# Optimization experiments

Measured on AMD Instinct MI355X. Metric: run time of the kernel, lower is better.

Reference implementation:

```python
import jax, jax.numpy as jnp
import numpy as np

V, D, L, H, T_BLK, DFF = 50257, 768, 12, 12, 1024, 4096
DK = D // H
LN_EPS = 1e-5


def setup_inputs() -> dict:
    key = jax.random.key(0)
    ks = jax.random.split(key, 16)
    s = 0.02
    inp = {
        "idx": jax.random.randint(ks[0], (2, 1024), 0, V),
        "tok_emb": jax.random.normal(ks[1], (V, D), jnp.float32) * s,
        "pos_emb": jax.random.normal(ks[2], (1, T_BLK, D), jnp.float32) * s,
        "ln1_w": jnp.ones((L, D), jnp.float32),
        "ln1_b": jnp.zeros((L, D), jnp.float32),
        "qkv_w": jax.random.normal(ks[3], (L, 3 * D, D), jnp.float32) * s,
        "qkv_b": jnp.zeros((L, 3 * D), jnp.float32),
        "proj_w": jax.random.normal(ks[4], (L, D, D), jnp.float32) * s,
        "proj_b": jnp.zeros((L, D), jnp.float32),
        "ln2_w": jnp.ones((L, D), jnp.float32),
        "ln2_b": jnp.zeros((L, D), jnp.float32),
        "ff1_w": jax.random.normal(ks[5], (L, DFF, D), jnp.float32) * s,
        "ff1_b": jnp.zeros((L, DFF), jnp.float32),
        "ff2_w": jax.random.normal(ks[6], (L, D, DFF), jnp.float32) * s,
        "ff2_b": jnp.zeros((L, D), jnp.float32),
        "lnf_w": jnp.ones((D,), jnp.float32),
        "lnf_b": jnp.zeros((D,), jnp.float32),
        "head_w": jax.random.normal(ks[7], (V, D), jnp.float32) * s,
    }
    return inp


def _layernorm(x, w, b):
    mu = jnp.mean(x, axis=-1, keepdims=True)
    var = jnp.var(x, axis=-1, keepdims=True)
    return (x - mu) * jax.lax.rsqrt(var + LN_EPS) * w + b


def _gpt_forward(idx, tok_emb, pos_emb, ln1_w, ln1_b, qkv_w, qkv_b, proj_w, proj_b,
                 ln2_w, ln2_b, ff1_w, ff1_b, ff2_w, ff2_b, lnf_w, lnf_b, head_w):
    B, T = idx.shape
    x = tok_emb[idx] + pos_emb[:, :T, :]  # [B,T,D]
    mask = jnp.tril(jnp.ones((T, T), bool))  # causal
    scale = 1.0 / np.sqrt(DK)

    def step(x, p):
        l1w, l1b, qw, qb, pw, pb, l2w, l2b, f1w, f1b, f2w, f2b = p
        h = _layernorm(x, l1w, l1b)
        qkv = h @ qw.T + qb  # [B,T,3D]
        q, k, v = jnp.split(qkv, 3, axis=-1)
        q = q.reshape(B, T, H, DK).transpose(0, 2, 1, 3)  # [B,H,T,DK]
        k = k.reshape(B, T, H, DK).transpose(0, 2, 1, 3)
        v = v.reshape(B, T, H, DK).transpose(0, 2, 1, 3)
        att = jnp.einsum('bhtd,bhsd->bhts', q, k) * scale
        att = jnp.where(mask, att, -jnp.inf)
        att = jax.nn.softmax(att, axis=-1)
        y = jnp.einsum('bhts,bhsd->bhtd', att, v)
        y = y.transpose(0, 2, 1, 3).reshape(B, T, D)
        x = x + y @ pw.T + pb
        h2 = _layernorm(x, l2w, l2b)
        ff = jax.nn.gelu(h2 @ f1w.T + f1b, approximate=False) @ f2w.T + f2b
        return x + ff, None

    params = (ln1_w, ln1_b, qkv_w, qkv_b, proj_w, proj_b,
              ln2_w, ln2_b, ff1_w, ff1_b, ff2_w, ff2_b)
    x, _ = jax.lax.scan(step, x, params)
    x = _layernorm(x, lnf_w, lnf_b)
    return x @ head_w.T  # [B,T,V] logits


def reference(idx, tok_emb, pos_emb, ln1_w, ln1_b, qkv_w, qkv_b, proj_w, proj_b,
              ln2_w, ln2_b, ff1_w, ff1_b, ff2_w, ff2_b, lnf_w, lnf_b, head_w):
    return _gpt_forward(idx, tok_emb, pos_emb, ln1_w, ln1_b, qkv_w, qkv_b, proj_w,
                        proj_b, ln2_w, ln2_b, ff1_w, ff1_b, ff2_w, ff2_b,
                        lnf_w, lnf_b, head_w)
```

## Files before the change

### kernel.cpp

```cpp
#include <hip/hip_runtime.h>
#include <hip/hip_bf16.h>
#include <math.h>

#define Dm 768
#define Tt 1024
#define Bb 2
#define Hh 12
#define DFF 4096
#define Ll 12
#define Vv 50257
#define ROWS (Bb*Tt)
#define LN_EPS 1e-5f

typedef unsigned int uint;
typedef unsigned short ushort;
typedef float f32x4 __attribute__((ext_vector_type(4)));
typedef short bf16x8 __attribute__((ext_vector_type(8)));
typedef ushort us8 __attribute__((ext_vector_type(8)));

__device__ __forceinline__ ushort f2bf(float f) {
  uint u = __builtin_bit_cast(uint, f);
  u += 0x7FFFu + ((u >> 16) & 1u);
  return (ushort)(u >> 16);
}

#define GLL(gp, lp)                                                          \
  __builtin_amdgcn_global_load_lds(                                          \
      (const __attribute__((address_space(1))) uint*)(gp),                   \
      (__attribute__((address_space(3))) uint*)(lp), 16, 0, 0)

__global__ __launch_bounds__(256) void embed_ln(
    const int* __restrict__ idx, const float* __restrict__ tok,
    const float* __restrict__ pos, const float* __restrict__ w,
    const float* __restrict__ b, float* __restrict__ x,
    ushort* __restrict__ out) {
  const int row = blockIdx.x;
  const int t = row & (Tt - 1);
  const int tid = threadIdx.x;
  const float* tsrc = tok + (size_t)idx[row] * Dm;
  const float* psrc = pos + (size_t)t * Dm;
  float v[3];
  float sum = 0.f, sq = 0.f;
#pragma unroll
  for (int i = 0; i < 3; i++) {
    const int d = tid + i * 256;
    v[i] = tsrc[d] + psrc[d];
    x[(size_t)row * Dm + d] = v[i];
    sum += v[i]; sq += v[i] * v[i];
  }
#pragma unroll
  for (int off = 32; off > 0; off >>= 1) {
    sum += __shfl_xor(sum, off);
    sq  += __shfl_xor(sq, off);
  }
  __shared__ float red[8];
  const int wid = tid >> 6, lane = tid & 63;
  if (lane == 0) { red[wid] = sum; red[wid + 4] = sq; }
  __syncthreads();
  sum = red[0] + red[1] + red[2] + red[3];
  sq  = red[4] + red[5] + red[6] + red[7];
  const float mu = sum * (1.f / Dm);
  const float var = sq * (1.f / Dm) - mu * mu;
  const float rstd = rsqrtf(var + LN_EPS);
  ushort* dst = out + (size_t)row * Dm;
#pragma unroll
  for (int i = 0; i < 3; i++) {
    const int d = tid + i * 256;
    dst[d] = f2bf((v[i] - mu) * rstd * w[d] + b[d]);
  }
}

__global__ __launch_bounds__(192) void red_ln(
    const float* __restrict__ part, int nsk, const float* __restrict__ bias,
    float* __restrict__ x, const float* __restrict__ w,
    const float* __restrict__ b, ushort* __restrict__ out) {
  const int row = blockIdx.x;
  const int tid = threadIdx.x;
  const size_t o4 = (size_t)row * 192 + tid;
  float4 xv = ((const float4*)x)[o4];
  const float4 b4 = ((const float4*)bias)[tid];
  xv.x += b4.x; xv.y += b4.y; xv.z += b4.z; xv.w += b4.w;
  for (int k = 0; k < nsk; k++) {
    const float4 p = ((const float4*)part)[(size_t)k * ROWS * 192 + o4];
    xv.x += p.x; xv.y += p.y; xv.z += p.z; xv.w += p.w;
  }
  ((float4*)x)[o4] = xv;
  float sum = xv.x + xv.y + xv.z + xv.w;
  float sq = xv.x * xv.x + xv.y * xv.y + xv.z * xv.z + xv.w * xv.w;
#pragma unroll
  for (int off = 32; off > 0; off >>= 1) {
    sum += __shfl_xor(sum, off);
    sq  += __shfl_xor(sq, off);
  }
  __shared__ float red[6];
  const int wid = tid >> 6, lane = tid & 63;
  if (lane == 0) { red[wid] = sum; red[wid + 3] = sq; }
  __syncthreads();
  sum = red[0] + red[1] + red[2];
  sq  = red[3] + red[4] + red[5];
  const float mu = sum * (1.f / Dm);
  const float var = sq * (1.f / Dm) - mu * mu;
  const float rstd = rsqrtf(var + LN_EPS);
  const float4 w4 = ((const float4*)w)[tid];
  const float4 bb4 = ((const float4*)b)[tid];
  ushort4 o;
  o.x = f2bf((xv.x - mu) * rstd * w4.x + bb4.x);
  o.y = f2bf((xv.y - mu) * rstd * w4.y + bb4.y);
  o.z = f2bf((xv.z - mu) * rstd * w4.z + bb4.z);
  o.w = f2bf((xv.w - mu) * rstd * w4.w + bb4.w);
  ((ushort4*)out)[o4] = o;
}

__global__ __launch_bounds__(256) void convert_w(
    const float* __restrict__ s, ushort* __restrict__ d, int n4) {
  const int stride = gridDim.x * 256;
  for (int i = blockIdx.x * 256 + threadIdx.x; i < n4; i += stride) {
    const float4 v = ((const float4*)s)[i];
    ushort4 o;
    o.x = f2bf(v.x); o.y = f2bf(v.y); o.z = f2bf(v.z); o.w = f2bf(v.w);
    ((ushort4*)d)[i] = o;
  }
}

#define EPI_QKV 0
#define EPI_PART 1
#define EPI_BIAS_GELU 2
#define EPI_NONE 3

template <int EPI>
__global__ __launch_bounds__(256) void gemm_mfma(
    const ushort* __restrict__ A, const ushort* __restrict__ B,
    const float* __restrict__ bias, void* __restrict__ Cv,
    void* __restrict__ Cv2, int Kloop, int Kstr, int Nloc, int ldC) {
  __shared__ char lds[32768];
  const int tid = threadIdx.x;
  const int l = tid & 63;
  const int wid = __builtin_amdgcn_readfirstlane(tid >> 6);
  const int wr = wid >> 1, wc = wid & 1;
  const int m0 = blockIdx.y * 128;
  const int n0 = blockIdx.x * 128;
  const int z = (EPI == EPI_PART) ? blockIdx.z : 0;
  if (EPI == EPI_PART) { A += (size_t)z * Kloop; B += (size_t)z * Kloop; }

  const int cperm = (((l & 3) ^ ((l >> 3) & 3)) * 8);
  const ushort* gA = A + (size_t)(m0 + wid * 32 + (l >> 2)) * Kstr + cperm;
  int rB = n0 + wid * 32 + (l >> 2);
  rB = min(rB, Nloc - 1);
  const ushort* gB = B + (size_t)rB * Kstr + cperm;

  const int rdSw = (l & 15) * 64 + (((l >> 4) ^ ((l >> 1) & 3)) * 16);
  const int aRd = wr * 4096 + rdSw;
  const int bRd = 8192 + wc * 4096 + rdSw;

  f32x4 acc[4][4] = {};
  const int nt = Kloop / 32;

  {
    const int lb = wid * 2048;
    GLL(gA, lds + lb);          GLL(gA + 16 * Kstr, lds + lb + 1024);
    GLL(gB, lds + 8192 + lb);   GLL(gB + 16 * Kstr, lds + 8192 + lb + 1024);
  }

  for (int t = 0; t < nt; ++t) {
    __syncthreads();
    if (t + 1 < nt) {
      const int base = ((t + 1) & 1) * 16384;
      const int lb = base + wid * 2048;
      const ushort* a = gA + (t + 1) * 32;
      const ushort* b = gB + (t + 1) * 32;
      GLL(a, lds + lb);         GLL(a + 16 * Kstr, lds + lb + 1024);
      GLL(b, lds + 8192 + lb);  GLL(b + 16 * Kstr, lds + 8192 + lb + 1024);
    }
    const int base = (t & 1) * 16384;
    bf16x8 av[4], bv[4];
#pragma unroll
    for (int i = 0; i < 4; ++i) {
      av[i] = *(const bf16x8*)(lds + base + aRd + i * 1024);
      bv[i] = *(const bf16x8*)(lds + base + bRd + i * 1024);
    }
#pragma unroll
    for (int i = 0; i < 4; ++i)
#pragma unroll
      for (int j = 0; j < 4; ++j)
        acc[i][j] = __builtin_amdgcn_mfma_f32_16x16x32_bf16(
            av[i], bv[j], acc[i][j], 0, 0, 0);
  }

#pragma unroll
  for (int fm = 0; fm < 4; ++fm) {
    const int row0 = m0 + wr * 64 + fm * 16 + (l >> 4) * 4;
#pragma unroll
    for (int fn = 0; fn < 4; ++fn) {
      const int col = n0 + wc * 64 + fn * 16 + (l & 15);
      if (col >= Nloc) continue;
      float bi = 0.f;
      if (EPI == EPI_QKV || EPI == EPI_BIAS_GELU) bi = bias[col];
      if (EPI == EPI_QKV && col >= 2 * Dm) {
        const int hh = (col - 2 * Dm) >> 6, dd = col & 63;
        const int bI = row0 >> 10, t0 = row0 & (Tt - 1);
        ushort4 o4;
        o4.x = f2bf(acc[fm][fn][0] + bi);
        o4.y = f2bf(acc[fm][fn][1] + bi);
        o4.z = f2bf(acc[fm][fn][2] + bi);
        o4.w = f2bf(acc[fm][fn][3] + bi);
        *(ushort4*)((ushort*)Cv2 +
                    ((size_t)((bI * Hh + hh) * 64 + dd)) * Tt + t0) = o4;
        continue;
      }
#pragma unroll
      for (int r = 0; r < 4; ++r) {
        float v = acc[fm][fn][r] + bi;
        const size_t off = (size_t)(row0 + r) * ldC + col;
        if (EPI == EPI_BIAS_GELU) {
          v = 0.5f * v * (1.f + erff(v * 0.70710678118654752f));
          ((ushort*)Cv)[off] = f2bf(v);
        } else if (EPI == EPI_QKV) {
          ((ushort*)Cv)[off] = f2bf(v);
        } else if (EPI == EPI_PART) {
          ((float*)Cv)[(size_t)z * ROWS * ldC + off] = v;
        } else {
          ((float*)Cv)[off] = v;
        }
      }
    }
  }
}

__global__ __launch_bounds__(512, 2) void gemm_head8(
    const ushort* __restrict__ A, const ushort* __restrict__ B,
    float* __restrict__ C) {
  __shared__ char lds[131072];
  const int tid = threadIdx.x;
  const int l = tid & 63;
  const int wid = __builtin_amdgcn_readfirstlane(tid >> 6);
  const int wm = wid >> 2, wn = wid & 3;

  const int bid = blockIdx.x;
  const int swz = (bid & 7) * 197 + (bid >> 3);
  const int pan = swz >> 3, mrw = swz & 7;
  const int m0 = mrw * 256;
  const int n0 = pan * 256;

  const ushort* gA[2];
  const ushort* gB[2];
#pragma unroll
  for (int j = 0; j < 2; j++) {
    const int c = tid + j * 512;
    const int r = c >> 2, kq = c & 3;
    gA[j] = A + (size_t)(m0 + r) * Dm + ((kq ^ ((r >> 1) & 3)) * 8);
    int rb = n0 + r;
    rb = min(rb, Vv - 1);
    gB[j] = B + (size_t)rb * Dm + ((kq ^ ((r >> 1) & 3)) * 8);
  }

#define HSTAGE(t)                                                            \
  do {                                                                       \
    char* _lb = lds + ((t) & 3) * 32768;                                     \
    const int _o = (t) * 32;                                                 \
    GLL(gA[0] + _o, _lb + tid * 16);                                         \
    GLL(gA[1] + _o, _lb + 8192 + tid * 16);                                  \
    GLL(gB[0] + _o, _lb + 16384 + tid * 16);                                 \
    GLL(gB[1] + _o, _lb + 24576 + tid * 16);                                 \
  } while (0)

  f32x4 acc[8][4] = {};
  const int s = l & 15, g = l >> 4;

  int aOff[8], bOff[4];
#pragma unroll
  for (int fm = 0; fm < 8; fm++) {
    const int r = wm * 128 + fm * 16 + s;
    aOff[fm] = r * 64 + ((g ^ ((r >> 1) & 3)) * 16);
  }
#pragma unroll
  for (int fn = 0; fn < 4; fn++) {
    const int r = wn * 64 + fn * 16 + s;
    bOff[fn] = 16384 + r * 64 + ((g ^ ((r >> 1) & 3)) * 16);
  }

  HSTAGE(0); HSTAGE(1); HSTAGE(2);
  asm volatile("s_waitcnt vmcnt(8)" ::: "memory");
  __builtin_amdgcn_s_barrier();
  __builtin_amdgcn_sched_barrier(0);

#define HITER(t, VC)                                                         \
  {                                                                          \
    if ((t) + 3 < 24) HSTAGE((t) + 3);                                       \
    char* bb = lds + ((t) & 3) * 32768;                                      \
    bf16x8 av[8], bv[4];                                                     \
    _Pragma("unroll")                                                        \
    for (int fm = 0; fm < 8; fm++) av[fm] = *(const bf16x8*)(bb + aOff[fm]); \
    _Pragma("unroll")                                                        \
    for (int fn = 0; fn < 4; fn++) bv[fn] = *(const bf16x8*)(bb + bOff[fn]); \
    __builtin_amdgcn_s_setprio(1);                                           \
    _Pragma("unroll")                                                        \
    for (int fm = 0; fm < 8; fm++)                                           \
      _Pragma("unroll")                                                      \
      for (int fn = 0; fn < 4; fn++)                                         \
        acc[fm][fn] = __builtin_amdgcn_mfma_f32_16x16x32_bf16(               \
            av[fm], bv[fn], acc[fm][fn], 0, 0, 0);                           \
    __builtin_amdgcn_s_setprio(0);                                           \
    asm volatile("s_waitcnt lgkmcnt(0)" ::: "memory");                       \
    asm volatile("s_waitcnt vmcnt(" #VC ")" ::: "memory");                   \
    __builtin_amdgcn_s_barrier();                                            \
    __builtin_amdgcn_sched_barrier(0);                                       \
  }

#pragma unroll 1
  for (int t = 0; t <= 20; ++t) HITER(t, 8);
  HITER(21, 4);
  HITER(22, 0);
  HITER(23, 0);

#pragma unroll
  for (int fm = 0; fm < 8; ++fm) {
    const int row0 = m0 + wm * 128 + fm * 16 + g * 4;
#pragma unroll
    for (int fn = 0; fn < 4; ++fn) {
      const int col = n0 + wn * 64 + fn * 16 + s;
      if (col >= Vv) continue;
#pragma unroll
      for (int r = 0; r < 4; ++r)
        C[(size_t)(row0 + r) * Vv + col] = acc[fm][fn][r];
    }
  }
}

__global__ __launch_bounds__(128) void attn_mfma(
    const ushort* __restrict__ qkv, const ushort* __restrict__ vTg,
    ushort* __restrict__ y) {
  __shared__ char lds[36864];
  const int tid = threadIdx.x;
  const int l = tid & 63;
  const int w = tid >> 6;
  const int s = l & 15, g = l >> 4;
  const int bq = gridDim.x - 1 - blockIdx.x;
  const int h = blockIdx.y, b = blockIdx.z;
  const int bh = b * Hh + h;

  const int qrow = bq * 32 + w * 16 + s;
  const ushort* qp = qkv + (size_t)(b * Tt + qrow) * 2304 + h * 64 + g * 8;
  const bf16x8 aq0 = *(const bf16x8*)qp;
  const bf16x8 aq1 = *(const bf16x8*)(qp + 32);

  size_t gofs[8];
#pragma unroll
  for (int i = 0; i < 8; i++) {
    const int c = tid + i * 128;
    if (i < 4) {
      const int kr = c >> 3;
      gofs[i] = (size_t)(b * Tt + kr) * 2304 + Dm + h * 64 + ((c & 7) ^ (kr & 7)) * 8;
    } else {
      const int cv = c - 512;
      const int vr = cv >> 3;
      gofs[i] = (size_t)(bh * 64 + vr) * Tt + ((cv & 7) ^ (vr & 7)) * 8;
    }
  }

#define ASTAGE(kt, base)                                                     \
  do {                                                                       \
    _Pragma("unroll")                                                        \
    for (int i = 0; i < 8; i++) {                                            \
      const ushort* p = (i < 4) ? (qkv + gofs[i] + (size_t)(kt) * 147456)    \
                                : (vTg + gofs[i] + (kt) * 64);               \
      GLL(p, lds + (base) + tid * 16 + i * 2048);                            \
    }                                                                        \
  } while (0)

  f32x4 oc[4] = {};
  float mrun[4], lrun[4];
#pragma unroll
  for (int r = 0; r < 4; r++) { mrun[r] = -INFINITY; lrun[r] = 0.f; }

  const int pB = 32768 + w * 2048;
  const int kSw = (s & 7);
  const int nkt = (bq >> 1) + 1;

  ASTAGE(0, 0);
  for (int kt = 0; kt < nkt; ++kt) {
    __syncthreads();
    if (kt + 1 < nkt) ASTAGE(kt + 1, ((kt + 1) & 1) * 16384);
    const int cur = (kt & 1) * 16384;

    f32x4 sc[4];
    __builtin_amdgcn_s_setprio(1);
#pragma unroll
    for (int jn = 0; jn < 4; jn++) {
      const int krow = cur + (jn * 16 + s) * 128;
      const bf16x8 bk0 = *(const bf16x8*)(lds + krow + ((g ^ kSw) * 16));
      const bf16x8 bk1 = *(const bf16x8*)(lds + krow + (((4 + g) ^ kSw) * 16));
      f32x4 z = {};
      z = __builtin_amdgcn_mfma_f32_16x16x32_bf16(aq0, bk0, z, 0, 0, 0);
      z = __builtin_amdgcn_mfma_f32_16x16x32_bf16(aq1, bk1, z, 0, 0, 0);
      sc[jn] = z;
    }
    __builtin_amdgcn_s_setprio(0);

    float cr[4];
    const bool diag = (kt == nkt - 1);
#pragma unroll
    for (int r = 0; r < 4; r++) {
      const int rowg = bq * 32 + w * 16 + g * 4 + r;
      float v[4];
#pragma unroll
      for (int jn = 0; jn < 4; jn++) {
        v[jn] = sc[jn][r] * 0.125f;
        if (diag && (kt * 64 + jn * 16 + s) > rowg) v[jn] = -INFINITY;
      }
      float mx = fmaxf(fmaxf(v[0], v[1]), fmaxf(v[2], v[3]));
      mx = fmaxf(mx, __shfl_xor(mx, 1));
      mx = fmaxf(mx, __shfl_xor(mx, 2));
      mx = fmaxf(mx, __shfl_xor(mx, 4));
      mx = fmaxf(mx, __shfl_xor(mx, 8));
      const float mnew = fmaxf(mrun[r], mx);
      const float corr = __expf(mrun[r] - mnew);
      mrun[r] = mnew;
      float ps = 0.f;
#pragma unroll
      for (int jn = 0; jn < 4; jn++) {
        const float p = __expf(v[jn] - mnew);
        ps += p;
        *(ushort*)(lds + pB + (g * 4 + r) * 128 +
                   (((2 * jn + (s >> 3)) ^ g) * 16) + (s & 7) * 2) = f2bf(p);
      }
      ps += __shfl_xor(ps, 1);
      ps += __shfl_xor(ps, 2);
      ps += __shfl_xor(ps, 4);
      ps += __shfl_xor(ps, 8);
      lrun[r] = lrun[r] * corr + ps;
      cr[r] = corr;
    }

    const float c01 = (s & 1) ? cr[1] : cr[0];
    const float c23 = (s & 1) ? cr[3] : cr[2];
    const float csel = (s & 2) ? c23 : c01;
    const float ccol = __shfl(csel, ((s >> 2) << 4) | s);
#pragma unroll
    for (int fm = 0; fm < 4; fm++) {
      oc[fm][0] *= ccol; oc[fm][1] *= ccol;
      oc[fm][2] *= ccol; oc[fm][3] *= ccol;
    }

    const bf16x8 bp0 = *(const bf16x8*)(lds + pB + s * 128 + ((g ^ (s >> 2)) * 16));
    const bf16x8 bp1 = *(const bf16x8*)(lds + pB + s * 128 + (((4 + g) ^ (s >> 2)) * 16));
    __builtin_amdgcn_s_setprio(1);
#pragma unroll
    for (int fm = 0; fm < 4; fm++) {
      const int vrow = cur + 8192 + (fm * 16 + s) * 128;
      const bf16x8 av0 = *(const bf16x8*)(lds + vrow + ((g ^ kSw) * 16));
      const bf16x8 av1 = *(const bf16x8*)(lds + vrow + (((4 + g) ^ kSw) * 16));
      oc[fm] = __builtin_amdgcn_mfma_f32_16x16x32_bf16(av0, bp0, oc[fm], 0, 0, 0);
      oc[fm] = __builtin_amdgcn_mfma_f32_16x16x32_bf16(av1, bp1, oc[fm], 0, 0, 0);
    }
    __builtin_amdgcn_s_setprio(0);
  }

  float li[4];
#pragma unroll
  for (int r = 0; r < 4; r++) li[r] = 1.f / lrun[r];
  const float l01 = (s & 1) ? li[1] : li[0];
  const float l23 = (s & 1) ? li[3] : li[2];
  const float lsel = (s & 2) ? l23 : l01;
  const float lcol = __shfl(lsel, ((s >> 2) << 4) | s);
  ushort* yp = y + (size_t)(b * Tt + qrow) * Dm + h * 64;
#pragma unroll
  for (int fm = 0; fm < 4; fm++) {
    ushort4 o4;
    o4.x = f2bf(oc[fm][0] * lcol);
    o4.y = f2bf(oc[fm][1] * lcol);
    o4.z = f2bf(oc[fm][2] * lcol);
    o4.w = f2bf(oc[fm][3] * lcol);
    *(ushort4*)(yp + fm * 16 + g * 4) = o4;
  }
}

extern "C" void kernel_launch(void* const* d_in, const int* in_sizes, int n_in,
                              void* d_out, int out_size, void* d_ws, size_t ws_size,
                              hipStream_t stream) {
  const int* idx = (const int*)d_in[0];
  const float* tok = (const float*)d_in[1];
  const float* pos = (const float*)d_in[2];
  const float* ln1w = (const float*)d_in[3];
  const float* ln1b = (const float*)d_in[4];
  const float* qkvw = (const float*)d_in[5];
  const float* qkvb = (const float*)d_in[6];
  const float* projw = (const float*)d_in[7];
  const float* projb = (const float*)d_in[8];
  const float* ln2w = (const float*)d_in[9];
  const float* ln2b = (const float*)d_in[10];
  const float* ff1w = (const float*)d_in[11];
  const float* ff1b = (const float*)d_in[12];
  const float* ff2w = (const float*)d_in[13];
  const float* ff2b = (const float*)d_in[14];
  const float* lnfw = (const float*)d_in[15];
  const float* lnfb = (const float*)d_in[16];
  const float* headw = (const float*)d_in[17];
  float* out = (float*)d_out;

  char* ws = (char*)d_ws;
  ushort* h    = (ushort*)ws;
  float*  x    = (float*)(ws + 3145728);
  ushort* y    = (ushort*)(ws + 9437184);
  ushort* qkv  = (ushort*)(ws + 12582912);
  ushort* vTg  = (ushort*)(ws + 22020096);
  ushort* ff   = (ushort*)(ws + 25165824);
  ushort* wb   = (ushort*)(ws + 41943040);
  float* projPart = (float*)(ws + 326755840);
  float* ff2Part  = (float*)(ws + 351921664);

  const size_t oPROJ = (size_t)Ll * 3 * Dm * Dm;
  const size_t oFF1  = oPROJ + (size_t)Ll * Dm * Dm;
  const size_t oFF2  = oFF1 + (size_t)Ll * DFF * Dm;
  const size_t oHEAD = oFF2 + (size_t)Ll * Dm * DFF;

  convert_w<<<2048, 256, 0, stream>>>(qkvw, wb, (int)(oPROJ / 4));
  convert_w<<<2048, 256, 0, stream>>>(projw, wb + oPROJ, (int)((oFF1 - oPROJ) / 4));
  convert_w<<<2048, 256, 0, stream>>>(ff1w, wb + oFF1, (int)((oFF2 - oFF1) / 4));
  convert_w<<<2048, 256, 0, stream>>>(ff2w, wb + oFF2, (int)((oHEAD - oFF2) / 4));
  convert_w<<<2048, 256, 0, stream>>>(headw, wb + oHEAD, (int)((size_t)Vv * Dm / 4));

  embed_ln<<<ROWS, 256, 0, stream>>>(idx, tok, pos, ln1w, ln1b, x, h);

  for (int l = 0; l < Ll; l++) {
    gemm_mfma<EPI_QKV><<<dim3(18, 16), 256, 0, stream>>>(
        h, wb + (size_t)l * 3 * Dm * Dm, qkvb + l * 3 * Dm, qkv, vTg,
        Dm, Dm, 3 * Dm, 3 * Dm);
    attn_mfma<<<dim3(32, Hh, Bb), 128, 0, stream>>>(qkv, vTg, y);
    gemm_mfma<EPI_PART><<<dim3(6, 16, 4), 256, 0, stream>>>(
        y, wb + oPROJ + (size_t)l * Dm * Dm, nullptr, projPart, nullptr,
        Dm / 4, Dm, Dm, Dm);
    red_ln<<<ROWS, 192, 0, stream>>>(projPart, 4, projb + l * Dm, x,
                                     ln2w + l * Dm, ln2b + l * Dm, h);
    gemm_mfma<EPI_BIAS_GELU><<<dim3(32, 16), 256, 0, stream>>>(
        h, wb + oFF1 + (size_t)l * DFF * Dm, ff1b + l * DFF, ff, nullptr,
        Dm, Dm, DFF, DFF);
    gemm_mfma<EPI_PART><<<dim3(6, 16, 4), 256, 0, stream>>>(
        ff, wb + oFF2 + (size_t)l * Dm * DFF, nullptr, ff2Part, nullptr,
        DFF / 4, DFF, Dm, Dm);
    const float* nw = (l == Ll - 1) ? lnfw : ln1w + (l + 1) * Dm;
    const float* nb = (l == Ll - 1) ? lnfb : ln1b + (l + 1) * Dm;
    red_ln<<<ROWS, 192, 0, stream>>>(ff2Part, 4, ff2b + l * Dm, x, nw, nb, h);
  }

  gemm_head8<<<1576, 512, 0, stream>>>(h, wb + oHEAD, out);
}
```

Before: 2.069 ms.

## Restructure LM-head GEMM into K=64 double-buffered stages with phased loads

Rewrites the vocabulary-head GEMM main loop to use K=64 tiles in a two-stage LDS buffer, with a new 128-byte-row XOR swizzle. Each k-tile is split into four phases that interleave LDS fragment reads, async global-to-LDS staging of the next tiles, and MFMA bursts between barriers. The aim is better overlap of memory traffic with matrix math and fewer loop iterations. In exchange it adds more barriers per tile and tighter vmcnt bookkeeping, which risks stalls or subtle hazards.

New measurement: 2.055 ms. No clear change (-0.7%).

```diff
diff --git a/kernel.cpp b/kernel.cpp
--- a/kernel.cpp
+++ b/kernel.cpp
@@ -28,6 +28,8 @@
   __builtin_amdgcn_global_load_lds(                                          \
       (const __attribute__((address_space(1))) uint*)(gp),                   \
       (__attribute__((address_space(3))) uint*)(lp), 16, 0, 0)
+
+#define MF(a, b, c) __builtin_amdgcn_mfma_f32_16x16x32_bf16(a, b, c, 0, 0, 0)
 
 __global__ __launch_bounds__(256) void embed_ln(
     const int* __restrict__ idx, const float* __restrict__ tok,
@@ -182,8 +184,7 @@
     for (int i = 0; i < 4; ++i)
 #pragma unroll
       for (int j = 0; j < 4; ++j)
-        acc[i][j] = __builtin_amdgcn_mfma_f32_16x16x32_bf16(
-            av[i], bv[j], acc[i][j], 0, 0, 0);
+        acc[i][j] = MF(av[i], bv[j], acc[i][j]);
   }
 
 #pragma unroll
@@ -234,6 +235,7 @@
   const int l = tid & 63;
   const int wid = __builtin_amdgcn_readfirstlane(tid >> 6);
   const int wm = wid >> 2, wn = wid & 3;
+  const int s = l & 15, g = l >> 4;
 
   const int bid = blockIdx.x;
   const int swz = (bid & 7) * 197 + (bid >> 3);
@@ -241,76 +243,91 @@
   const int m0 = mrw * 256;
   const int n0 = pan * 256;
 
-  const ushort* gA[2];
-  const ushort* gB[2];
-#pragma unroll
-  for (int j = 0; j < 2; j++) {
-    const int c = tid + j * 512;
-    const int r = c >> 2, kq = c & 3;
-    gA[j] = A + (size_t)(m0 + r) * Dm + ((kq ^ ((r >> 1) & 3)) * 8);
-    int rb = n0 + r;
-    rb = min(rb, Vv - 1);
-    gB[j] = B + (size_t)rb * Dm + ((kq ^ ((r >> 1) & 3)) * 8);
-  }
-
-#define HSTAGE(t)                                                            \
-  do {                                                                       \
-    char* _lb = lds + ((t) & 3) * 32768;                                     \
-    const int _o = (t) * 32;                                                 \
-    GLL(gA[0] + _o, _lb + tid * 16);                                         \
-    GLL(gA[1] + _o, _lb + 8192 + tid * 16);                                  \
-    GLL(gB[0] + _o, _lb + 16384 + tid * 16);                                 \
-    GLL(gB[1] + _o, _lb + 24576 + tid * 16);                                 \
-  } while (0)
+  const int r0 = tid >> 3;
+  const int q0 = (tid & 7) ^ (r0 & 7);
+  const ushort* pA0 = A + (size_t)(m0 + r0) * Dm + q0 * 8;
+  const ushort* pA1 = pA0 + (size_t)64 * Dm;
+  const ushort* pB[2][2];
+  pB[0][0] = B + (size_t)min(n0 + r0, Vv - 1) * Dm + q0 * 8;
+  pB[0][1] = B + (size_t)min(n0 + 64 + r0, Vv - 1) * Dm + q0 * 8;
+  pB[1][0] = B + (size_t)min(n0 + 128 + r0, Vv - 1) * Dm + q0 * 8;
+  pB[1][1] = B + (size_t)min(n0 + 192 + r0, Vv - 1) * Dm + q0 * 8;
+
+#define STG_A(t, h) do { if ((t) < 12) {                                     \
+    char* _d = lds + ((((t) & 1) * 2 + (h)) * 16384);                        \
+    GLL(pA0 + (size_t)(h) * 98304 + (t) * 64, _d + tid * 16);                \
+    GLL(pA1 + (size_t)(h) * 98304 + (t) * 64, _d + 8192 + tid * 16);         \
+  }} while (0)
+#define STG_B(t, h) do { if ((t) < 12) {                                     \
+    char* _d = lds + 65536 + ((((t) & 1) * 2 + (h)) * 16384);                \
+    GLL(pB[h][0] + (t) * 64, _d + tid * 16);                                 \
+    GLL(pB[h][1] + (t) * 64, _d + 8192 + tid * 16);                          \
+  }} while (0)
+
+  const int aK0 = ((0 * 4 + g) ^ (s & 7)) * 16;
+  const int aK1 = ((1 * 4 + g) ^ (s & 7)) * 16;
+  const int aBase = wm * 16384 + s * 128;
+  const int bBase = 65536 + (wn >> 1) * 16384 + (wn & 1) * 8192 + s * 128;
 
   f32x4 acc[8][4] = {};
-  const int s = l & 15, g = l >> 4;
-
-  int aOff[8], bOff[4];
-#pragma unroll
-  for (int fm = 0; fm < 8; fm++) {
-    const int r = wm * 128 + fm * 16 + s;
-    aOff[fm] = r * 64 + ((g ^ ((r >> 1) & 3)) * 16);
-  }
-#pragma unroll
-  for (int fn = 0; fn < 4; fn++) {
-    const int r = wn * 64 + fn * 16 + s;
-    bOff[fn] = 16384 + r * 64 + ((g ^ ((r >> 1) & 3)) * 16);
-  }
-
-  HSTAGE(0); HSTAGE(1); HSTAGE(2);
-  asm volatile("s_waitcnt vmcnt(8)" ::: "memory");
-  __builtin_amdgcn_s_barrier();
-  __builtin_amdgcn_sched_barrier(0);
-
-#define HITER(t, VC)                                                         \
+  bf16x8 bv[4][2];
+
+#define PH(t, p, STAGES, VMC)                                                \
   {                                                                          \
-    if ((t) + 3 < 24) HSTAGE((t) + 3);                                       \
-    char* bb = lds + ((t) & 3) * 32768;                                      \
-    bf16x8 av[8], bv[4];                                                     \
-    _Pragma("unroll")                                                        \
-    for (int fm = 0; fm < 8; fm++) av[fm] = *(const bf16x8*)(bb + aOff[fm]); \
-    _Pragma("unroll")                                                        \
-    for (int fn = 0; fn < 4; fn++) bv[fn] = *(const bf16x8*)(bb + bOff[fn]); \
+    const int cur = ((t) & 1) * 32768;                                       \
+    if ((p) == 1) {                                                          \
+      _Pragma("unroll")                                                      \
+      for (int fn = 0; fn < 4; fn++) {                                       \
+        bv[fn][0] = *(const bf16x8*)(lds + cur + bBase + fn * 2048 + aK0);   \
+        bv[fn][1] = *(const bf16x8*)(lds + cur + bBase + fn * 2048 + aK1);   \
+      }                                                                      \
+    }                                                                        \
+    bf16x8 a00 = *(const bf16x8*)(lds + cur + aBase + (2*(p)-2)*2048 + aK0); \
+    bf16x8 a01 = *(const bf16x8*)(lds + cur + aBase + (2*(p)-2)*2048 + aK1); \
+    bf16x8 a10 = *(const bf16x8*)(lds + cur + aBase + (2*(p)-1)*2048 + aK0); \
+    bf16x8 a11 = *(const bf16x8*)(lds + cur + aBase + (2*(p)-1)*2048 + aK1); \
+    STAGES;                                                                  \
+    __builtin_amdgcn_s_barrier();                                            \
+    asm volatile("s_waitcnt lgkmcnt(0)" ::: "memory");                       \
+    __builtin_amdgcn_sched_barrier(0);                                       \
     __builtin_amdgcn_s_setprio(1);                                           \
     _Pragma("unroll")                                                        \
-    for (int fm = 0; fm < 8; fm++)                                           \
-      _Pragma("unroll")                                                      \
-      for (int fn = 0; fn < 4; fn++)                                         \
-        acc[fm][fn] = __builtin_amdgcn_mfma_f32_16x16x32_bf16(               \
-            av[fm], bv[fn], acc[fm][fn], 0, 0, 0);                           \
+    for (int fn = 0; fn < 4; fn++) {                                         \
+      acc[2*(p)-2][fn] = MF(a00, bv[fn][0], acc[2*(p)-2][fn]);               \
+      acc[2*(p)-2][fn] = MF(a01, bv[fn][1], acc[2*(p)-2][fn]);               \
+      acc[2*(p)-1][fn] = MF(a10, bv[fn][0], acc[2*(p)-1][fn]);               \
+      acc[2*(p)-1][fn] = MF(a11, bv[fn][1], acc[2*(p)-1][fn]);               \
+    }                                                                        \
     __builtin_amdgcn_s_setprio(0);                                           \
-    asm volatile("s_waitcnt lgkmcnt(0)" ::: "memory");                       \
-    asm volatile("s_waitcnt vmcnt(" #VC ")" ::: "memory");                   \
+    VMC;                                                                     \
     __builtin_amdgcn_s_barrier();                                            \
-    __builtin_amdgcn_sched_barrier(0);                                       \
-  }
+  }
+
+  STG_B(0, 0); STG_B(0, 1); STG_A(0, 0); STG_A(0, 1); STG_B(1, 0); STG_B(1, 1);
+  asm volatile("s_waitcnt vmcnt(4)" ::: "memory");
+  __builtin_amdgcn_s_barrier();
 
 #pragma unroll 1
-  for (int t = 0; t <= 20; ++t) HITER(t, 8);
-  HITER(21, 4);
-  HITER(22, 0);
-  HITER(23, 0);
+  for (int i = 0; i < 6; ++i) {
+    const int t0 = 2 * i, t1 = 2 * i + 1, t2 = 2 * i + 2, t3 = 2 * i + 3;
+    PH(t0, 1, { STG_A(t1, 0); }, {});
+    PH(t0, 2, { STG_A(t1, 1); STG_B(t2, 0); }, {});
+    PH(t0, 3, { STG_B(t2, 1); }, {});
+    if (i < 5) {
+      PH(t0, 4, {}, { asm volatile("s_waitcnt vmcnt(4)" ::: "memory"); });
+    } else {
+      PH(t0, 4, {}, { asm volatile("s_waitcnt vmcnt(0)" ::: "memory"); });
+    }
+    PH(t1, 1, { STG_A(t2, 0); }, {});
+    PH(t1, 2, { STG_A(t2, 1); }, {});
+    PH(t1, 3, { STG_B(t3, 0); }, {});
+    if (i < 5) {
+      PH(t1, 4, { STG_B(t3, 1); },
+         { asm volatile("s_waitcnt vmcnt(4)" ::: "memory"); });
+    } else {
+      PH(t1, 4, {}, {});
+    }
+  }
 
 #pragma unroll
   for (int fm = 0; fm < 8; ++fm) {
@@ -324,6 +341,9 @@
         C[(size_t)(row0 + r) * Vv + col] = acc[fm][fn][r];
     }
   }
+#undef PH
+#undef STG_A
+#undef STG_B
 }
 
 __global__ __launch_bounds__(128) void attn_mfma(
@@ -390,8 +410,8 @@
       const bf16x8 bk0 = *(const bf16x8*)(lds + krow + ((g ^ kSw) * 16));
       const bf16x8 bk1 = *(const bf16x8*)(lds + krow + (((4 + g) ^ kSw) * 16));
       f32x4 z = {};
-      z = __builtin_amdgcn_mfma_f32_16x16x32_bf16(aq0, bk0, z, 0, 0, 0);
-      z = __builtin_amdgcn_mfma_f32_16x16x32_bf16(aq1, bk1, z, 0, 0, 0);
+      z = MF(aq0, bk0, z);
+      z = MF(aq1, bk1, z);
       sc[jn] = z;
     }
     __builtin_amdgcn_s_setprio(0);
@@ -449,8 +469,8 @@
       const int vrow = cur + 8192 + (fm * 16 + s) * 128;
       const bf16x8 av0 = *(const bf16x8*)(lds + vrow + ((g ^ kSw) * 16));
       const bf16x8 av1 = *(const bf16x8*)(lds + vrow + (((4 + g) ^ kSw) * 16));
-      oc[fm] = __builtin_amdgcn_mfma_f32_16x16x32_bf16(av0, bp0, oc[fm], 0, 0, 0);
-      oc[fm] = __builtin_amdgcn_mfma_f32_16x16x32_bf16(av1, bp1, oc[fm], 0, 0, 0);
+      oc[fm] = MF(av0, bp0, oc[fm]);
+      oc[fm] = MF(av1, bp1, oc[fm]);
     }
     __builtin_amdgcn_s_setprio(0);
   }
```
